# Optimization experiments

Measured on AMD Instinct MI355X. Metric: run time of the kernel, lower is better.

Reference implementation:

```python
import jax, jax.numpy as jnp
import numpy as np

N_POINTS = 8388608  # 8M points


def setup_inputs() -> dict:
    key = jax.random.key(0)
    k1, k2 = jax.random.split(key)
    pcloud = jax.random.normal(k1, (1, N_POINTS, 3), dtype=jnp.float32)
    P1 = jax.random.normal(k2, (3,), dtype=jnp.float32)
    return {"pcloud": pcloud, "P1": P1, "K": 64}


def reference(pcloud, P1, K):
    # pcloud: (1, N, 3) -> (N, 3); P1: (3,) -> (1, 3)
    pts = pcloud.reshape(-1, 3)
    diff = pts - P1.reshape(1, 3)
    dist = jnp.sqrt(jnp.sum(diff * diff, axis=1))  # L2 distance per point, (N,)
    # torch.topk(largest=False) == top_k on negated distances
    _, idx = jax.lax.top_k(-dist, K)  # (K,)
    return pts[idx], idx.reshape(1, -1)
```

## Files before the change

kernel.cpp:

```cpp
#include <hip/hip_runtime.h>
#include <stdint.h>

#define NBINS 4096
#define NB2   4096
#define NBLK  2048
#define SLOT  16
#define OVF_CAP 8192
#define LDS_CAND 8192
#define SAMP_PTS 131072
#define SBLK 128
#define CHUNK_PTS 256
#define CHUNK_F4  192

typedef const __attribute__((address_space(1))) void* gas_ptr;
typedef __attribute__((address_space(3))) void* las_ptr;

__device__ __forceinline__ uint32_t dist_key(float x, float y, float z,
                                             float px, float py, float pz) {
    float dx = __fsub_rn(x, px);
    float dy = __fsub_rn(y, py);
    float dz = __fsub_rn(z, pz);
    float s = __fadd_rn(__fadd_rn(__fmul_rn(dx, dx), __fmul_rn(dy, dy)),
                        __fmul_rn(dz, dz));
    float d = __fsqrt_rn(s);
    return __float_as_uint(d);
}

__global__ void __launch_bounds__(256) sample_scan_kernel(
        const float* __restrict__ pts, const float* __restrict__ P1,
        uint32_t* __restrict__ ghist, uint32_t* __restrict__ cutp,
        uint32_t* __restrict__ done_s, int nsamp, int K) {
    __shared__ uint32_t lh[NBINS];
    __shared__ uint32_t ssum[256];
    __shared__ int is_last;
    for (int i = threadIdx.x; i < NBINS; i += 256) lh[i] = 0;
    __syncthreads();
    float px = P1[0], py = P1[1], pz = P1[2];
    int gid = blockIdx.x * 256 + threadIdx.x;
    const float4* p4 = (const float4*)pts;
    if (gid * 4 < nsamp) {
        float4 A = p4[gid * 3 + 0];
        float4 Bv = p4[gid * 3 + 1];
        float4 Cv = p4[gid * 3 + 2];
        atomicAdd(&lh[dist_key(A.x, A.y, A.z, px, py, pz) >> 20], 1u);
        atomicAdd(&lh[dist_key(A.w, Bv.x, Bv.y, px, py, pz) >> 20], 1u);
        atomicAdd(&lh[dist_key(Bv.z, Bv.w, Cv.x, px, py, pz) >> 20], 1u);
        atomicAdd(&lh[dist_key(Cv.y, Cv.z, Cv.w, px, py, pz) >> 20], 1u);
    }
    __syncthreads();
    for (int i = threadIdx.x; i < NBINS; i += 256) {
        uint32_t v = lh[i];
        if (v) atomicAdd(&ghist[i], v);
    }
    __syncthreads();
    if (threadIdx.x == 0) {
        asm volatile("s_waitcnt vmcnt(0)" ::: "memory");
        uint32_t old = __hip_atomic_fetch_add(done_s, 1u, __ATOMIC_RELAXED,
                                              __HIP_MEMORY_SCOPE_AGENT);
        is_last = (old == (uint32_t)(gridDim.x - 1));
    }
    __syncthreads();
    if (!is_last) return;

    int t = threadIdx.x;
    uint32_t mine[16];
    uint32_t local = 0;
    for (int j = 0; j < 16; ++j) {
        mine[j] = __hip_atomic_load(&ghist[t * 16 + j], __ATOMIC_RELAXED,
                                    __HIP_MEMORY_SCOPE_AGENT);
        local += mine[j];
    }
    ssum[t] = local;
    __syncthreads();
    for (int off = 1; off < 256; off <<= 1) {
        uint32_t v = (t >= off) ? ssum[t - off] : 0;
        __syncthreads();
        ssum[t] += v;
        __syncthreads();
    }
    uint32_t incl = ssum[t];
    uint32_t excl = incl - local;
    if (excl < (uint32_t)K && incl >= (uint32_t)K) {
        uint32_t run = excl;
        for (int j = 0; j < 16; ++j) {
            run += mine[j];
            if (run >= (uint32_t)K) { *cutp = (uint32_t)(t * 16 + j); break; }
        }
    }
}

__global__ void __launch_bounds__(256) filter_kernel(
        const float* __restrict__ pts, const float* __restrict__ P1,
        const uint32_t* __restrict__ cutp,
        unsigned long long* __restrict__ gslots,
        uint32_t* __restrict__ gcount,
        uint32_t* __restrict__ ovf_cnt, unsigned long long* __restrict__ ovf,
        int nchunks, int N) {
    __shared__ float4 ring[4][3][CHUNK_F4];
    __shared__ unsigned long long lhits[SLOT];
    __shared__ uint32_t lcnt;
    if (threadIdx.x == 0) lcnt = 0;
    __syncthreads();

    const float4* p4 = (const float4*)pts;
    float px = P1[0], py = P1[1], pz = P1[2];
    uint32_t cb = *cutp;
    int w = threadIdx.x >> 6;
    int lane = threadIdx.x & 63;
    int b = blockIdx.x;
    int cpb = (nchunks + NBLK - 1) / NBLK;
    int cbeg = b * cpb;
    int cend = cbeg + cpb; if (cend > nchunks) cend = nchunks;

    int tiles = 0;
    if (cend > cbeg + w) tiles = (cend - (cbeg + w) + 3) / 4;

    auto stage = [&](int buf, int i) {
        const float4* s = p4 + (size_t)(cbeg + w + 4 * i) * CHUNK_F4 + lane;
        float4* d = &ring[w][buf][0];
        __builtin_amdgcn_global_load_lds((gas_ptr)(s),       (las_ptr)(d),       16, 0, 0);
        __builtin_amdgcn_global_load_lds((gas_ptr)(s + 64),  (las_ptr)(d + 64),  16, 0, 0);
        __builtin_amdgcn_global_load_lds((gas_ptr)(s + 128), (las_ptr)(d + 128), 16, 0, 0);
    };

    if (tiles > 0) stage(0, 0);
    if (tiles > 1) stage(1, 1);

    for (int i = 0; i < tiles; ++i) {
        if (i + 2 < tiles) stage((i + 2) % 3, i + 2);
        if (i + 2 < tiles)      asm volatile("s_waitcnt vmcnt(6)" ::: "memory");
        else if (i + 1 < tiles) asm volatile("s_waitcnt vmcnt(3)" ::: "memory");
        else                    asm volatile("s_waitcnt vmcnt(0)" ::: "memory");
        __builtin_amdgcn_sched_barrier(0);

        const float* fb = (const float*)&ring[w][i % 3][0] + lane * 12;
        float4 A  = *(const float4*)(fb);
        float4 Bv = *(const float4*)(fb + 4);
        float4 Cv = *(const float4*)(fb + 8);
        uint32_t kk[4];
        kk[0] = dist_key(A.x, A.y, A.z, px, py, pz);
        kk[1] = dist_key(A.w, Bv.x, Bv.y, px, py, pz);
        kk[2] = dist_key(Bv.z, Bv.w, Cv.x, px, py, pz);
        kk[3] = dist_key(Cv.y, Cv.z, Cv.w, px, py, pz);
        uint32_t pbase = (uint32_t)(cbeg + w + 4 * i) * CHUNK_PTS + (uint32_t)lane * 4;
        #pragma unroll
        for (int j = 0; j < 4; ++j) {
            if ((kk[j] >> 20) <= cb) {
                unsigned long long cv = ((unsigned long long)kk[j] << 32) |
                                        (unsigned long long)(pbase + j);
                uint32_t pos = atomicAdd(&lcnt, 1u);
                if (pos < SLOT) lhits[pos] = cv;
                else {
                    uint32_t op = atomicAdd(ovf_cnt, 1u);
                    if (op < OVF_CAP) ovf[op] = cv;
                }
            }
        }
    }
    if (b == NBLK - 1 && threadIdx.x == 0) {
        for (int i = nchunks * CHUNK_PTS; i < N; ++i) {
            uint32_t kk = dist_key(pts[3 * i], pts[3 * i + 1], pts[3 * i + 2], px, py, pz);
            if ((kk >> 20) <= cb) {
                unsigned long long cv = ((unsigned long long)kk << 32) |
                                        (unsigned long long)(uint32_t)i;
                uint32_t pos = atomicAdd(&lcnt, 1u);
                if (pos < SLOT) lhits[pos] = cv;
                else {
                    uint32_t op = atomicAdd(ovf_cnt, 1u);
                    if (op < OVF_CAP) ovf[op] = cv;
                }
            }
        }
    }
    __syncthreads();
    uint32_t n = lcnt; if (n > SLOT) n = SLOT;
    if (threadIdx.x < n) gslots[(size_t)b * SLOT + threadIdx.x] = lhits[threadIdx.x];
    if (threadIdx.x == 0) gcount[b] = n;
}

__global__ void __launch_bounds__(1024) refine_select_kernel(
        const uint32_t* __restrict__ gcount,
        const unsigned long long* __restrict__ gslots,
        const uint32_t* __restrict__ ovf_cnt,
        const unsigned long long* __restrict__ ovf,
        const uint32_t* __restrict__ cutp,
        unsigned long long* __restrict__ cand2,
        const float* __restrict__ pts,
        float* __restrict__ out, int K) {
    __shared__ uint32_t hist2[NB2];
    __shared__ uint32_t ssum[1024];
    __shared__ unsigned long long lcand[LDS_CAND];
    __shared__ uint32_t cut2_s, m2_s;
    int t = threadIdx.x;
    uint32_t cb = *cutp;
    unsigned long long R = ((unsigned long long)(cb + 1)) << 20;
    uint32_t M32 = (uint32_t)((((unsigned long long)NB2) << 32) / R);
    uint32_t novf = *ovf_cnt; if (novf > OVF_CAP) novf = OVF_CAP;

    for (int i = t; i < NB2; i += 1024) hist2[i] = 0;
    if (t == 0) { m2_s = 0; cut2_s = NB2 - 1; }
    __syncthreads();
    for (int b = t; b < NBLK; b += 1024) {
        uint32_t n = gcount[b]; if (n > SLOT) n = SLOT;
        for (uint32_t j = 0; j < n; ++j) {
            uint32_t key = (uint32_t)(gslots[(size_t)b * SLOT + j] >> 32);
            atomicAdd(&hist2[(uint32_t)(((unsigned long long)key * M32) >> 32)], 1u);
        }
    }
    for (uint32_t i = t; i < novf; i += 1024) {
        uint32_t key = (uint32_t)(ovf[i] >> 32);
        atomicAdd(&hist2[(uint32_t)(((unsigned long long)key * M32) >> 32)], 1u);
    }
    __syncthreads();

    uint32_t mine[4];
    uint32_t local = 0;
    for (int j = 0; j < 4; ++j) { mine[j] = hist2[t * 4 + j]; local += mine[j]; }
    ssum[t] = local;
    __syncthreads();
    for (int off = 1; off < 1024; off <<= 1) {
        uint32_t v = (t >= off) ? ssum[t - off] : 0;
        __syncthreads();
        ssum[t] += v;
        __syncthreads();
    }
    uint32_t incl = ssum[t], excl = incl - local;
    if (excl < (uint32_t)K && incl >= (uint32_t)K) {
        uint32_t run = excl;
        for (int j = 0; j < 4; ++j) {
            run += mine[j];
            if (run >= (uint32_t)K) { cut2_s = (uint32_t)(t * 4 + j); break; }
        }
    }
    __syncthreads();
    uint32_t c2 = cut2_s;

    for (int b = t; b < NBLK; b += 1024) {
        uint32_t n = gcount[b]; if (n > SLOT) n = SLOT;
        for (uint32_t j = 0; j < n; ++j) {
            unsigned long long cv = gslots[(size_t)b * SLOT + j];
            uint32_t key = (uint32_t)(cv >> 32);
            if ((uint32_t)(((unsigned long long)key * M32) >> 32) <= c2) {
                uint32_t pos = atomicAdd(&m2_s, 1u);
                if (pos < LDS_CAND) lcand[pos] = cv;
                cand2[pos] = cv;
            }
        }
    }
    for (uint32_t i = t; i < novf; i += 1024) {
        unsigned long long cv = ovf[i];
        uint32_t key = (uint32_t)(cv >> 32);
        if ((uint32_t)(((unsigned long long)key * M32) >> 32) <= c2) {
            uint32_t pos = atomicAdd(&m2_s, 1u);
            if (pos < LDS_CAND) lcand[pos] = cv;
            cand2[pos] = cv;
        }
    }
    __syncthreads();
    uint32_t M2 = m2_s;

    if (M2 <= LDS_CAND) {
        for (uint32_t i = t; i < M2; i += 1024) {
            unsigned long long ci = lcand[i];
            uint32_t rank = 0;
            for (uint32_t j = 0; j < M2; ++j) rank += (lcand[j] < ci) ? 1u : 0u;
            if (rank < (uint32_t)K) {
                uint32_t idx = (uint32_t)(ci & 0xFFFFFFFFu);
                out[3 * rank + 0] = pts[3 * idx + 0];
                out[3 * rank + 1] = pts[3 * idx + 1];
                out[3 * rank + 2] = pts[3 * idx + 2];
                out[3 * K + rank] = (float)idx;
            }
        }
    } else {
        for (uint32_t i = t; i < M2; i += 1024) {
            unsigned long long ci = cand2[i];
            uint32_t rank = 0;
            for (uint32_t j = 0; j < M2; ++j) rank += (cand2[j] < ci) ? 1u : 0u;
            if (rank < (uint32_t)K) {
                uint32_t idx = (uint32_t)(ci & 0xFFFFFFFFu);
                out[3 * rank + 0] = pts[3 * idx + 0];
                out[3 * rank + 1] = pts[3 * idx + 1];
                out[3 * rank + 2] = pts[3 * idx + 2];
                out[3 * K + rank] = (float)idx;
            }
        }
    }
}

extern "C" void kernel_launch(void* const* d_in, const int* in_sizes, int n_in,
                              void* d_out, int out_size, void* d_ws, size_t ws_size,
                              hipStream_t stream) {
    const float* pts = (const float*)d_in[0];
    const float* P1  = (const float*)d_in[1];
    float* out = (float*)d_out;

    int N = in_sizes[0] / 3;
    int nchunks = N / CHUNK_PTS;
    int K = out_size / 4;
    int nsamp = (N < SAMP_PTS) ? (N / 4) * 4 : SAMP_PTS;

    uint32_t* w       = (uint32_t*)d_ws;
    uint32_t* ovf_cnt = w + 0;
    uint32_t* cutp    = w + 1;
    uint32_t* done_s  = w + 2;
    uint32_t* hist    = w + 4;
    uint32_t* gcount  = w + 4 + NBINS;
    unsigned long long* gslots = (unsigned long long*)(w + 4 + NBINS + NBLK);
    unsigned long long* ovf    = gslots + (size_t)NBLK * SLOT;
    unsigned long long* cand2  = ovf + OVF_CAP;

    hipMemsetAsync(w, 0, (size_t)(4 + NBINS) * sizeof(uint32_t), stream);
    sample_scan_kernel<<<SBLK, 256, 0, stream>>>(pts, P1, hist, cutp, done_s, nsamp, K);
    filter_kernel<<<NBLK, 256, 0, stream>>>(pts, P1, cutp, gslots, gcount,
                                            ovf_cnt, ovf, nchunks, N);
    refine_select_kernel<<<1, 1024, 0, stream>>>(gcount, gslots, ovf_cnt, ovf,
                                                 cutp, cand2, pts, out, K);
}
```

Before: 47.19 us.

## Replace LDS-staged triple-buffered loads with direct per-thread global float4 loads

The filter kernel no longer stages point data through a per-wave LDS ring with global_load_lds and manual vmcnt waits. Each thread now reads three float4 values straight from global memory per 1024-point tile, with tiles split contiguously across blocks. This drops the LDS traffic, the ring buffers and the explicit pipeline bookkeeping, and it raises occupancy since LDS use falls. In exchange, the per-thread loads are strided by 48 bytes, so coalescing is weaker, and latency hiding now relies on the hardware and compiler rather than explicit prefetch.

```diff
diff --git a/kernel.cpp b/kernel.cpp
--- a/kernel.cpp
+++ b/kernel.cpp
@@ -9,11 +9,8 @@
 #define LDS_CAND 8192
 #define SAMP_PTS 131072
 #define SBLK 128
-#define CHUNK_PTS 256
-#define CHUNK_F4  192
-
-typedef const __attribute__((address_space(1))) void* gas_ptr;
-typedef __attribute__((address_space(3))) void* las_ptr;
+#define TILE_PTS 1024
+#define TILE_F4  768
 
 __device__ __forceinline__ uint32_t dist_key(float x, float y, float z,
                                              float px, float py, float pz) {
@@ -95,8 +92,7 @@
         unsigned long long* __restrict__ gslots,
         uint32_t* __restrict__ gcount,
         uint32_t* __restrict__ ovf_cnt, unsigned long long* __restrict__ ovf,
-        int nchunks, int N) {
-    __shared__ float4 ring[4][3][CHUNK_F4];
+        int ntiles, int N) {
     __shared__ unsigned long long lhits[SLOT];
     __shared__ uint32_t lcnt;
     if (threadIdx.x == 0) lcnt = 0;
@@ -105,44 +101,22 @@
     const float4* p4 = (const float4*)pts;
     float px = P1[0], py = P1[1], pz = P1[2];
     uint32_t cb = *cutp;
-    int w = threadIdx.x >> 6;
-    int lane = threadIdx.x & 63;
     int b = blockIdx.x;
-    int cpb = (nchunks + NBLK - 1) / NBLK;
-    int cbeg = b * cpb;
-    int cend = cbeg + cpb; if (cend > nchunks) cend = nchunks;
-
-    int tiles = 0;
-    if (cend > cbeg + w) tiles = (cend - (cbeg + w) + 3) / 4;
-
-    auto stage = [&](int buf, int i) {
-        const float4* s = p4 + (size_t)(cbeg + w + 4 * i) * CHUNK_F4 + lane;
-        float4* d = &ring[w][buf][0];
-        __builtin_amdgcn_global_load_lds((gas_ptr)(s),       (las_ptr)(d),       16, 0, 0);
-        __builtin_amdgcn_global_load_lds((gas_ptr)(s + 64),  (las_ptr)(d + 64),  16, 0, 0);
-        __builtin_amdgcn_global_load_lds((gas_ptr)(s + 128), (las_ptr)(d + 128), 16, 0, 0);
-    };
-
-    if (tiles > 0) stage(0, 0);
-    if (tiles > 1) stage(1, 1);
-
-    for (int i = 0; i < tiles; ++i) {
-        if (i + 2 < tiles) stage((i + 2) % 3, i + 2);
-        if (i + 2 < tiles)      asm volatile("s_waitcnt vmcnt(6)" ::: "memory");
-        else if (i + 1 < tiles) asm volatile("s_waitcnt vmcnt(3)" ::: "memory");
-        else                    asm volatile("s_waitcnt vmcnt(0)" ::: "memory");
-        __builtin_amdgcn_sched_barrier(0);
-
-        const float* fb = (const float*)&ring[w][i % 3][0] + lane * 12;
-        float4 A  = *(const float4*)(fb);
-        float4 Bv = *(const float4*)(fb + 4);
-        float4 Cv = *(const float4*)(fb + 8);
+    int tpb = (ntiles + NBLK - 1) / NBLK;
+    int tbeg = b * tpb;
+    int tend = tbeg + tpb; if (tend > ntiles) tend = ntiles;
+
+    for (int tl = tbeg; tl < tend; ++tl) {
+        const float4* s = p4 + (size_t)tl * TILE_F4 + 3 * threadIdx.x;
+        float4 A  = s[0];
+        float4 Bv = s[1];
+        float4 Cv = s[2];
         uint32_t kk[4];
         kk[0] = dist_key(A.x, A.y, A.z, px, py, pz);
         kk[1] = dist_key(A.w, Bv.x, Bv.y, px, py, pz);
         kk[2] = dist_key(Bv.z, Bv.w, Cv.x, px, py, pz);
         kk[3] = dist_key(Cv.y, Cv.z, Cv.w, px, py, pz);
-        uint32_t pbase = (uint32_t)(cbeg + w + 4 * i) * CHUNK_PTS + (uint32_t)lane * 4;
+        uint32_t pbase = (uint32_t)tl * TILE_PTS + (uint32_t)threadIdx.x * 4;
         #pragma unroll
         for (int j = 0; j < 4; ++j) {
             if ((kk[j] >> 20) <= cb) {
@@ -158,7 +132,7 @@
         }
     }
     if (b == NBLK - 1 && threadIdx.x == 0) {
-        for (int i = nchunks * CHUNK_PTS; i < N; ++i) {
+        for (int i = ntiles * TILE_PTS; i < N; ++i) {
             uint32_t kk = dist_key(pts[3 * i], pts[3 * i + 1], pts[3 * i + 2], px, py, pz);
             if ((kk >> 20) <= cb) {
                 unsigned long long cv = ((unsigned long long)kk << 32) |
@@ -296,7 +270,7 @@
     float* out = (float*)d_out;
 
     int N = in_sizes[0] / 3;
-    int nchunks = N / CHUNK_PTS;
+    int ntiles = N / TILE_PTS;
     int K = out_size / 4;
     int nsamp = (N < SAMP_PTS) ? (N / 4) * 4 : SAMP_PTS;
 
@@ -313,7 +287,7 @@
     hipMemsetAsync(w, 0, (size_t)(4 + NBINS) * sizeof(uint32_t), stream);
     sample_scan_kernel<<<SBLK, 256, 0, stream>>>(pts, P1, hist, cutp, done_s, nsamp, K);
     filter_kernel<<<NBLK, 256, 0, stream>>>(pts, P1, cutp, gslots, gcount,
-                                            ovf_cnt, ovf, nchunks, N);
+                                            ovf_cnt, ovf, ntiles, N);
     refine_select_kernel<<<1, 1024, 0, stream>>>(gcount, gslots, ovf_cnt, ovf,
                                                  cutp, cand2, pts, out, K);
 }
```

New measurement: 46.45 us. Within noise of the previous version (-1.6%).

## Replace async global-to-LDS triple-buffer ring with register prefetch and LDS transpose

Applied to the files above, without the earlier changes.

The filter kernel no longer uses a three-deep ring of direct global-to-LDS loads with manual vmcnt waits. Each wave now loads the next chunk into registers while processing the current one, staged through a single per-wave LDS buffer to re-shuffle the AoS layout. This cuts LDS footprint, which may allow more resident blocks, but leaves only one chunk of prefetch in flight and adds an explicit register-to-LDS store. There is also no barrier between the LDS reads of one iteration and the next iteration's overwrite, relying on in-order execution within a wave.

```diff
diff --git a/kernel.cpp b/kernel.cpp
--- a/kernel.cpp
+++ b/kernel.cpp
@@ -11,9 +11,6 @@
 #define SBLK 128
 #define CHUNK_PTS 256
 #define CHUNK_F4  192
-
-typedef const __attribute__((address_space(1))) void* gas_ptr;
-typedef __attribute__((address_space(3))) void* las_ptr;
 
 __device__ __forceinline__ uint32_t dist_key(float x, float y, float z,
                                              float px, float py, float pz) {
@@ -96,7 +93,7 @@
         uint32_t* __restrict__ gcount,
         uint32_t* __restrict__ ovf_cnt, unsigned long long* __restrict__ ovf,
         int nchunks, int N) {
-    __shared__ float4 ring[4][3][CHUNK_F4];
+    __shared__ float4 park[4][CHUNK_F4];
     __shared__ unsigned long long lhits[SLOT];
     __shared__ uint32_t lcnt;
     if (threadIdx.x == 0) lcnt = 0;
@@ -112,28 +109,23 @@
     int cbeg = b * cpb;
     int cend = cbeg + cpb; if (cend > nchunks) cend = nchunks;
 
-    int tiles = 0;
-    if (cend > cbeg + w) tiles = (cend - (cbeg + w) + 3) / 4;
-
-    auto stage = [&](int buf, int i) {
-        const float4* s = p4 + (size_t)(cbeg + w + 4 * i) * CHUNK_F4 + lane;
-        float4* d = &ring[w][buf][0];
-        __builtin_amdgcn_global_load_lds((gas_ptr)(s),       (las_ptr)(d),       16, 0, 0);
-        __builtin_amdgcn_global_load_lds((gas_ptr)(s + 64),  (las_ptr)(d + 64),  16, 0, 0);
-        __builtin_amdgcn_global_load_lds((gas_ptr)(s + 128), (las_ptr)(d + 128), 16, 0, 0);
-    };
-
-    if (tiles > 0) stage(0, 0);
-    if (tiles > 1) stage(1, 1);
-
-    for (int i = 0; i < tiles; ++i) {
-        if (i + 2 < tiles) stage((i + 2) % 3, i + 2);
-        if (i + 2 < tiles)      asm volatile("s_waitcnt vmcnt(6)" ::: "memory");
-        else if (i + 1 < tiles) asm volatile("s_waitcnt vmcnt(3)" ::: "memory");
-        else                    asm volatile("s_waitcnt vmcnt(0)" ::: "memory");
-        __builtin_amdgcn_sched_barrier(0);
-
-        const float* fb = (const float*)&ring[w][i % 3][0] + lane * 12;
+    float4 r0, r1, r2;
+    int c = cbeg + w;
+    if (c < cend) {
+        const float4* s = p4 + (size_t)c * CHUNK_F4;
+        r0 = s[lane]; r1 = s[lane + 64]; r2 = s[lane + 128];
+    }
+    for (; c < cend; c += 4) {
+        park[w][lane] = r0;
+        park[w][lane + 64] = r1;
+        park[w][lane + 128] = r2;
+        int cn = c + 4;
+        if (cn < cend) {
+            const float4* s = p4 + (size_t)cn * CHUNK_F4;
+            r0 = s[lane]; r1 = s[lane + 64]; r2 = s[lane + 128];
+        }
+        asm volatile("s_waitcnt lgkmcnt(0)" ::: "memory");
+        const float* fb = (const float*)&park[w][0] + lane * 12;
         float4 A  = *(const float4*)(fb);
         float4 Bv = *(const float4*)(fb + 4);
         float4 Cv = *(const float4*)(fb + 8);
@@ -142,7 +134,7 @@
         kk[1] = dist_key(A.w, Bv.x, Bv.y, px, py, pz);
         kk[2] = dist_key(Bv.z, Bv.w, Cv.x, px, py, pz);
         kk[3] = dist_key(Cv.y, Cv.z, Cv.w, px, py, pz);
-        uint32_t pbase = (uint32_t)(cbeg + w + 4 * i) * CHUNK_PTS + (uint32_t)lane * 4;
+        uint32_t pbase = (uint32_t)c * CHUNK_PTS + (uint32_t)lane * 4;
         #pragma unroll
         for (int j = 0; j < 4; ++j) {
             if ((kk[j] >> 20) <= cb) {
```

New measurement: 46.71 us. Within noise of the previous version (-1.0%).
